# Kernel tuning notes

Hardware: AMD Instinct MI355X
Metric: run time of the kernel (lower is better)

The kernel has to match this reference:

```python
import jax, jax.numpy as jnp
import numpy as np

B, N, F_IN, F_OUT = 4, 4096, 64, 64
ALPHA = 0.2   # leakyrelu negative slope
M_MIX = 0.8   # self.m
NEG_INF = -1e12


def setup_inputs() -> dict:
    key = jax.random.key(0)
    k1, k2, k3, k4 = jax.random.split(key, 4)
    inp = jax.random.normal(k1, (B, N, F_IN), dtype=jnp.float32)
    adj = jax.random.uniform(k2, (B, N, N), dtype=jnp.float32)
    # xavier_uniform with gain=1.414
    limW = 1.414 * np.sqrt(6.0 / (F_IN + F_OUT))
    W = jax.random.uniform(k3, (F_IN, F_OUT), dtype=jnp.float32, minval=-limW, maxval=limW)
    lima = 1.414 * np.sqrt(6.0 / (2 * F_OUT + 1))
    a = jax.random.uniform(k4, (2 * F_OUT, 1), dtype=jnp.float32, minval=-lima, maxval=lima)
    return {"inp": inp, "adj": adj, "W": W, "a": a}


def reference(inp, adj, W, a):
    # h: [B, N, F_OUT]
    h = jnp.einsum("bnf,fo->bno", inp, W)
    # The torch code builds a_input[b,i,j] = [h_i ; h_j], applies leakyrelu
    # elementwise, then contracts with a. Since leakyrelu is elementwise,
    # e[b,i,j] = lrelu(h_i) @ a[:F] + lrelu(h_j) @ a[F:], exactly.
    lh = jax.nn.leaky_relu(h, negative_slope=ALPHA)          # [B, N, F_OUT]
    f_src = lh @ a[:F_OUT, 0]                                # [B, N]  (h_i term)
    f_dst = lh @ a[F_OUT:, 0]                                # [B, N]  (h_j term)
    e = f_src[:, :, None] + f_dst[:, None, :]                # [B, N, N]
    dj = M_MIX * adj + (1.0 - M_MIX) * e
    attention = jnp.where(dj > 0, dj, NEG_INF)
    # torch softmax over dim=1 (the i axis)
    attention = jax.nn.softmax(attention, axis=1)
    # dropout is identity in eval mode
    h_prime = jnp.einsum("bij,bjo->bio", attention, h)       # [B, N, F_OUT]
    return jax.nn.relu(h_prime)
```

## Files before the change

### kernel.cpp

```cpp
#include <hip/hip_runtime.h>
#include <hip/hip_bf16.h>


#define Bn 4
#define Nn 4096

typedef _Float16 half8 __attribute__((ext_vector_type(8)));
typedef _Float16 half4 __attribute__((ext_vector_type(4)));
typedef float f32x4 __attribute__((ext_vector_type(4)));

__global__ __launch_bounds__(256) void k_prep(
    const float* __restrict__ inp, const float* __restrict__ W,
    const float* __restrict__ a, float* __restrict__ h,
    float* __restrict__ fsrc, float* __restrict__ fdst) {
  __shared__ float Ws[64 * 64];
  __shared__ float as[128];
  __shared__ float xs[4][64];
  const int t = threadIdx.x;
  for (int k = t; k < 4096; k += 256) Ws[k] = W[k];
  if (t < 128) as[t] = a[t];
  const int w = t >> 6;
  const int o = t & 63;
  const int row = blockIdx.x * 4 + w;
  xs[w][o] = inp[(size_t)row * 64 + o];
  __syncthreads();
  float acc = 0.f;
  const float* xr = xs[w];
#pragma unroll
  for (int f = 0; f < 64; ++f) acc += xr[f] * Ws[f * 64 + o];
  h[(size_t)row * 64 + o] = acc;
  float lh = acc > 0.f ? acc : 0.2f * acc;
  float vs = lh * as[o];
  float vd = lh * as[64 + o];
#pragma unroll
  for (int off = 32; off > 0; off >>= 1) {
    vs += __shfl_down(vs, off);
    vd += __shfl_down(vd, off);
  }
  if (o == 0) { fsrc[row] = vs; fdst[row] = vd; }
}

__global__ __launch_bounds__(256) void k_estats(
    const float* __restrict__ adj, const float* __restrict__ fsrc,
    const float* __restrict__ fdst, _Float16* __restrict__ E,
    float* __restrict__ s) {
  const int t = threadIdx.x;
  const int jb = blockIdx.x, ic = blockIdx.y, b = blockIdx.z;
  const int j = jb * 1024 + t * 4;
  const int i0 = ic * 64;
  __shared__ float fss[64];
  if (t < 64) fss[t] = fsrc[b * Nn + i0 + t];
  __syncthreads();
  const float4 fd = *(const float4*)&fdst[b * Nn + j];
  const float4* ap = (const float4*)(adj + ((size_t)(b * Nn + i0)) * Nn + j);
  _Float16* ep = E + ((size_t)(b * Nn + i0)) * Nn + j;
  float s0 = 0.f, s1 = 0.f, s2 = 0.f, s3 = 0.f;
#pragma unroll 4
  for (int ii = 0; ii < 64; ++ii) {
    float4 v = ap[(size_t)ii * 1024];
    float fi = fss[ii];
    float d0 = 0.8f * v.x + 0.2f * (fi + fd.x);
    float d1 = 0.8f * v.y + 0.2f * (fi + fd.y);
    float d2 = 0.8f * v.z + 0.2f * (fi + fd.z);
    float d3 = 0.8f * v.w + 0.2f * (fi + fd.w);
    float e0 = d0 > 0.f ? __expf(d0) : 0.f;
    float e1 = d1 > 0.f ? __expf(d1) : 0.f;
    float e2 = d2 > 0.f ? __expf(d2) : 0.f;
    float e3 = d3 > 0.f ? __expf(d3) : 0.f;
    s0 += e0; s1 += e1; s2 += e2; s3 += e3;
    half4 e;
    e[0] = (_Float16)e0; e[1] = (_Float16)e1;
    e[2] = (_Float16)e2; e[3] = (_Float16)e3;
    *(half4*)(ep + (size_t)ii * Nn) = e;
  }
  atomicAdd(&s[b * Nn + j + 0], s0);
  atomicAdd(&s[b * Nn + j + 1], s1);
  atomicAdd(&s[b * Nn + j + 2], s2);
  atomicAdd(&s[b * Nn + j + 3], s3);
}

__global__ __launch_bounds__(256) void k_hscale(
    const float* __restrict__ h, const float* __restrict__ s,
    _Float16* __restrict__ hT) {
  const int t = threadIdx.x;
  const int jt = blockIdx.x, b = blockIdx.y;
  __shared__ _Float16 hl[64][72];
#pragma unroll
  for (int r = 0; r < 4; ++r) {
    const int jl = r * 16 + (t >> 4);
    const int j = jt * 64 + jl;
    const int o4 = (t & 15) * 4;
    float sv = s[b * Nn + j];
    float si = sv > 0.f ? 1.0f / sv : 0.f;
    float4 hv = *(const float4*)&h[((size_t)(b * Nn + j)) * 64 + o4];
    hl[o4 + 0][jl] = (_Float16)(hv.x * si);
    hl[o4 + 1][jl] = (_Float16)(hv.y * si);
    hl[o4 + 2][jl] = (_Float16)(hv.z * si);
    hl[o4 + 3][jl] = (_Float16)(hv.w * si);
  }
  __syncthreads();
#pragma unroll
  for (int r = 0; r < 2; ++r) {
    const int o = r * 32 + (t >> 3);
    const int ch = t & 7;
    half8 v = *(half8*)&hl[o][ch * 8];
    *(half8*)&hT[((size_t)(b * 64 + o)) * 4096 + jt * 64 + ch * 8] = v;
  }
}

__global__ __launch_bounds__(256) void k_attnmm(
    const _Float16* __restrict__ E, const _Float16* __restrict__ hT,
    float* __restrict__ out) {
  const int t = threadIdx.x;
  const int ib = blockIdx.x;
  const int b = blockIdx.y;
  const int i0 = ib * 64;
  const int w = t >> 6;
  const int lane = t & 63;

  __shared__ _Float16 hs[64][264];

  f32x4 acc[4];
#pragma unroll
  for (int nt = 0; nt < 4; ++nt)
#pragma unroll
    for (int r = 0; r < 4; ++r) acc[nt][r] = 0.f;

  const int ai = i0 + w * 16 + (lane & 15);
  const int ko = (lane >> 4) * 8;
  const _Float16* Erow = E + ((size_t)(b * Nn + ai)) * Nn;
  const int so = t >> 2;
  const int sk = (t & 3) * 64;
  const _Float16* hTrow = hT + ((size_t)(b * 64 + so)) * Nn + sk;

  for (int ch = 0; ch < 16; ++ch) {
    const int k0 = ch * 256;
    __syncthreads();
#pragma unroll
    for (int q = 0; q < 8; ++q) {
      half8 v = *(const half8*)(hTrow + k0 + q * 8);
      *(half8*)&hs[so][sk + q * 8] = v;
    }
    __syncthreads();
#pragma unroll
    for (int kt = 0; kt < 8; ++kt) {
      half8 af = *(const half8*)(Erow + k0 + kt * 32 + ko);
#pragma unroll
      for (int nt = 0; nt < 4; ++nt) {
        half8 bf = *(const half8*)&hs[nt * 16 + (lane & 15)][kt * 32 + ko];
        acc[nt] = __builtin_amdgcn_mfma_f32_16x16x32_f16(af, bf, acc[nt], 0, 0, 0);
      }
    }
  }
#pragma unroll
  for (int nt = 0; nt < 4; ++nt)
#pragma unroll
    for (int r = 0; r < 4; ++r) {
      const int i = i0 + w * 16 + (lane >> 4) * 4 + r;
      const int o = nt * 16 + (lane & 15);
      out[((size_t)(b * Nn + i)) * 64 + o] = fmaxf(acc[nt][r], 0.f);
    }
}

extern "C" void kernel_launch(void* const* d_in, const int* in_sizes, int n_in,
                              void* d_out, int out_size, void* d_ws, size_t ws_size,
                              hipStream_t stream) {
  const float* inp = (const float*)d_in[0];
  const float* adj = (const float*)d_in[1];
  const float* W   = (const float*)d_in[2];
  const float* a   = (const float*)d_in[3];
  float* out = (float*)d_out;

  float* ws   = (float*)d_ws;
  float* h    = ws;
  float* fsrc = h + 1048576;
  float* fdst = fsrc + 16384;
  float* s    = fdst + 16384;
  _Float16* hT = (_Float16*)(s + 16384);
  _Float16* E  = hT + (size_t)1048576;

  hipMemsetAsync(s, 0, 16384 * sizeof(float), stream);
  k_prep<<<Bn * Nn / 4, 256, 0, stream>>>(inp, W, a, h, fsrc, fdst);
  k_estats<<<dim3(4, 64, Bn), 256, 0, stream>>>(adj, fsrc, fdst, E, s);
  k_hscale<<<dim3(64, Bn), 256, 0, stream>>>(h, s, hT);
  k_attnmm<<<dim3(64, Bn), 256, 0, stream>>>(E, hT, out);
}
```

Before: 475.6 us.

## Split-K the attention matmul and replace column-sum atomics with partial buffers

The attention-times-h matmul is split along K into four slices, so the grid grows from 256 to 1024 blocks, and a new reduction kernel sums the partials and applies ReLU. The column-sum atomics and the memset before them are replaced by per-row-chunk partial sums, which the hscale kernel adds up. The aim is better occupancy of the GPU's compute units for the MFMA stage and no atomic contention. In exchange it writes and reads about 16 MB of float partials and adds one more kernel launch.

```diff
diff --git a/kernel.cpp b/kernel.cpp
--- a/kernel.cpp
+++ b/kernel.cpp
@@ -4,6 +4,8 @@
 
 #define Bn 4
 #define Nn 4096
+#define KS 4
+#define IC 64
 
 typedef _Float16 half8 __attribute__((ext_vector_type(8)));
 typedef _Float16 half4 __attribute__((ext_vector_type(4)));
@@ -43,7 +45,7 @@
 __global__ __launch_bounds__(256) void k_estats(
     const float* __restrict__ adj, const float* __restrict__ fsrc,
     const float* __restrict__ fdst, _Float16* __restrict__ E,
-    float* __restrict__ s) {
+    float* __restrict__ pm) {
   const int t = threadIdx.x;
   const int jb = blockIdx.x, ic = blockIdx.y, b = blockIdx.z;
   const int j = jb * 1024 + t * 4;
@@ -73,25 +75,31 @@
     e[2] = (_Float16)e2; e[3] = (_Float16)e3;
     *(half4*)(ep + (size_t)ii * Nn) = e;
   }
-  atomicAdd(&s[b * Nn + j + 0], s0);
-  atomicAdd(&s[b * Nn + j + 1], s1);
-  atomicAdd(&s[b * Nn + j + 2], s2);
-  atomicAdd(&s[b * Nn + j + 3], s3);
+  float4 sv; sv.x = s0; sv.y = s1; sv.z = s2; sv.w = s3;
+  *(float4*)&pm[((size_t)(ic * Bn + b)) * Nn + j] = sv;
 }
 
 __global__ __launch_bounds__(256) void k_hscale(
-    const float* __restrict__ h, const float* __restrict__ s,
+    const float* __restrict__ h, const float* __restrict__ pm,
     _Float16* __restrict__ hT) {
   const int t = threadIdx.x;
   const int jt = blockIdx.x, b = blockIdx.y;
   __shared__ _Float16 hl[64][72];
+  __shared__ float sis[64];
+  if (t < 64) {
+    const int j = jt * 64 + t;
+    float sv = 0.f;
+#pragma unroll 8
+    for (int ic = 0; ic < IC; ++ic) sv += pm[((size_t)(ic * Bn + b)) * Nn + j];
+    sis[t] = sv > 0.f ? 1.0f / sv : 0.f;
+  }
+  __syncthreads();
 #pragma unroll
   for (int r = 0; r < 4; ++r) {
     const int jl = r * 16 + (t >> 4);
     const int j = jt * 64 + jl;
     const int o4 = (t & 15) * 4;
-    float sv = s[b * Nn + j];
-    float si = sv > 0.f ? 1.0f / sv : 0.f;
+    float si = sis[jl];
     float4 hv = *(const float4*)&h[((size_t)(b * Nn + j)) * 64 + o4];
     hl[o4 + 0][jl] = (_Float16)(hv.x * si);
     hl[o4 + 1][jl] = (_Float16)(hv.y * si);
@@ -110,11 +118,13 @@
 
 __global__ __launch_bounds__(256) void k_attnmm(
     const _Float16* __restrict__ E, const _Float16* __restrict__ hT,
-    float* __restrict__ out) {
-  const int t = threadIdx.x;
-  const int ib = blockIdx.x;
-  const int b = blockIdx.y;
+    float* __restrict__ part) {
+  const int t = threadIdx.x;
+  const int ks = blockIdx.x;
+  const int ib = blockIdx.y;
+  const int b = blockIdx.z;
   const int i0 = ib * 64;
+  const int kbase = ks * 1024;
   const int w = t >> 6;
   const int lane = t & 63;
 
@@ -128,12 +138,12 @@
 
   const int ai = i0 + w * 16 + (lane & 15);
   const int ko = (lane >> 4) * 8;
-  const _Float16* Erow = E + ((size_t)(b * Nn + ai)) * Nn;
+  const _Float16* Erow = E + ((size_t)(b * Nn + ai)) * Nn + kbase;
   const int so = t >> 2;
   const int sk = (t & 3) * 64;
-  const _Float16* hTrow = hT + ((size_t)(b * 64 + so)) * Nn + sk;
-
-  for (int ch = 0; ch < 16; ++ch) {
+  const _Float16* hTrow = hT + ((size_t)(b * 64 + so)) * Nn + kbase + sk;
+
+  for (int ch = 0; ch < 4; ++ch) {
     const int k0 = ch * 256;
     __syncthreads();
 #pragma unroll
@@ -158,8 +168,25 @@
     for (int r = 0; r < 4; ++r) {
       const int i = i0 + w * 16 + (lane >> 4) * 4 + r;
       const int o = nt * 16 + (lane & 15);
-      out[((size_t)(b * Nn + i)) * 64 + o] = fmaxf(acc[nt][r], 0.f);
+      part[(((size_t)ks * Bn + b) * Nn + i) * 64 + o] = acc[nt][r];
     }
+}
+
+__global__ __launch_bounds__(256) void k_final(
+    const float* __restrict__ part, float* __restrict__ out) {
+  const int e = blockIdx.x * 256 + threadIdx.x;
+  const float4* p4 = (const float4*)part;
+  float4 sv = p4[e];
+  const size_t stride = (size_t)Bn * Nn * 64 / 4;
+#pragma unroll
+  for (int ks = 1; ks < KS; ++ks) {
+    float4 v = p4[(size_t)ks * stride + e];
+    sv.x += v.x; sv.y += v.y; sv.z += v.z; sv.w += v.w;
+  }
+  float4 r;
+  r.x = fmaxf(sv.x, 0.f); r.y = fmaxf(sv.y, 0.f);
+  r.z = fmaxf(sv.z, 0.f); r.w = fmaxf(sv.w, 0.f);
+  ((float4*)out)[e] = r;
 }
 
 extern "C" void kernel_launch(void* const* d_in, const int* in_sizes, int n_in,
@@ -175,13 +202,14 @@
   float* h    = ws;
   float* fsrc = h + 1048576;
   float* fdst = fsrc + 16384;
-  float* s    = fdst + 16384;
-  _Float16* hT = (_Float16*)(s + 16384);
-  _Float16* E  = hT + (size_t)1048576;
-
-  hipMemsetAsync(s, 0, 16384 * sizeof(float), stream);
+  float* pm   = fdst + 16384;
+  float* part = pm + (size_t)IC * Bn * Nn;
+  _Float16* hT = (_Float16*)(part + (size_t)KS * Bn * Nn * 64);
+  _Float16* E  = hT + (size_t)Bn * 64 * Nn;
+
   k_prep<<<Bn * Nn / 4, 256, 0, stream>>>(inp, W, a, h, fsrc, fdst);
-  k_estats<<<dim3(4, 64, Bn), 256, 0, stream>>>(adj, fsrc, fdst, E, s);
-  k_hscale<<<dim3(64, Bn), 256, 0, stream>>>(h, s, hT);
-  k_attnmm<<<dim3(64, Bn), 256, 0, stream>>>(E, hT, out);
-}
+  k_estats<<<dim3(4, IC, Bn), 256, 0, stream>>>(adj, fsrc, fdst, E, pm);
+  k_hscale<<<dim3(64, Bn), 256, 0, stream>>>(h, pm, hT);
+  k_attnmm<<<dim3(KS, 64, Bn), 256, 0, stream>>>(E, hT, part);
+  k_final<<<Bn * Nn * 64 / 4 / 256, 256, 0, stream>>>(part, out);
+}
```

Measured after the change: 453.8 us. 4.6% less time.
